# Optimization experiments

Hardware: AMD Instinct MI355X
Metric: run time of the kernel (lower is better)

## Reference

```python
import jax, jax.numpy as jnp
import numpy as np

D_MODEL = 768
HEADS = 12
D_HEAD = D_MODEL // HEADS
D_DYNA = 768
EPS = 1e-5
B, SP, SI = 16, 256, 1024


def _layernorm(x, g, b):
    mu = jnp.mean(x, axis=-1, keepdims=True)
    var = jnp.var(x, axis=-1, keepdims=True)
    return (x - mu) * jax.lax.rsqrt(var + EPS) * g + b


def _mha(q, k, v, wq, bq, wk, bk, wv, bv, wo, bo):
    # weights stored [d_in, d_out]; torch Linear math y = x @ W^T + b is
    # equivalent with transposed storage.
    B_ = q.shape[0]
    qh = (q @ wq + bq).reshape(B_, -1, HEADS, D_HEAD)
    kh = (k @ wk + bk).reshape(B_, -1, HEADS, D_HEAD)
    vh = (v @ wv + bv).reshape(B_, -1, HEADS, D_HEAD)
    scores = jnp.einsum('bqhd,bkhd->bhqk', qh, kh) / np.sqrt(D_HEAD).astype(np.float32)
    attn = jax.nn.softmax(scores, axis=-1)  # dropout disabled (eval)
    out = jnp.einsum('bhqk,bkhd->bqhd', attn, vh).reshape(B_, -1, D_MODEL)
    return out @ wo + bo


def setup_inputs() -> dict:
    key = jax.random.key(0)
    ks = iter(jax.random.split(key, 40))
    s = 0.02
    d = {
        'image': jax.random.normal(next(ks), (B, SI, D_MODEL), jnp.float32),
        'prompt': jax.random.normal(next(ks), (B, SP, D_MODEL), jnp.float32),
        'posi': jax.random.normal(next(ks), (B, SI, D_MODEL), jnp.float32),
        'posp': jax.random.normal(next(ks), (B, SP, D_MODEL), jnp.float32),
    }
    for ln in ('ln_p1', 'ln_p2', 'ln_p3', 'ln_i1'):
        d[ln + '_g'] = jnp.ones((D_MODEL,), jnp.float32)
        d[ln + '_b'] = jnp.zeros((D_MODEL,), jnp.float32)
    for pre in ('pp', 'pi'):
        for nm in ('q', 'k', 'v', 'o'):
            d[f'{pre}_w{nm}'] = s * jax.random.normal(next(ks), (D_MODEL, D_MODEL), jnp.float32)
            d[f'{pre}_b{nm}'] = jnp.zeros((D_MODEL,), jnp.float32)
    d['ff_w1'] = s * jax.random.normal(next(ks), (D_MODEL, D_MODEL), jnp.float32)
    d['ff_b1'] = jnp.zeros((D_MODEL,), jnp.float32)
    d['ff_w2'] = s * jax.random.normal(next(ks), (D_MODEL, D_DYNA), jnp.float32)
    d['ff_b2'] = jnp.zeros((D_DYNA,), jnp.float32)
    return d


def reference(image, prompt, posi, posp,
              ln_p1_g, ln_p1_b, ln_p2_g, ln_p2_b, ln_p3_g, ln_p3_b, ln_i1_g, ln_i1_b,
              pp_wq, pp_bq, pp_wk, pp_bk, pp_wv, pp_bv, pp_wo, pp_bo,
              pi_wq, pi_bq, pi_wk, pi_bk, pi_wv, pi_bv, pi_wo, pi_bo,
              ff_w1, ff_b1, ff_w2, ff_b2):
    prompt0 = prompt + posp
    xp = _layernorm(prompt0, ln_p1_g, ln_p1_b)
    xp = _mha(xp, xp, xp, pp_wq, pp_bq, pp_wk, pp_bk, pp_wv, pp_bv, pp_wo, pp_bo)
    prompt = prompt + xp  # dropout_p1 is identity in eval
    xp = _layernorm(prompt + prompt0, ln_p2_g, ln_p2_b)
    xi = _layernorm(image + posi, ln_i1_g, ln_i1_b)
    xp = _mha(xp, xi, xi, pi_wq, pi_bq, pi_wk, pi_bk, pi_wv, pi_bv, pi_wo, pi_bo)
    prompt = prompt + xp  # dropout_p2 identity
    xp = _layernorm(prompt + prompt0, ln_p3_g, ln_p3_b)
    xp = jax.nn.relu(xp @ ff_w1 + ff_b1) @ ff_w2 + ff_b2
    return xp
```

## Files before the change

kernel.cpp:

```cpp
#include <hip/hip_runtime.h>
#include <hip/hip_bf16.h>
#include <stdint.h>
#include <math.h>

#define D_MODEL 768
#define HEADS 12
#define D_HEAD 64
#define BATCH 16
#define SP 256
#define SI 1024
#define NP (BATCH * SP)
#define NI (BATCH * SI)

#define GLOBAL_AS __attribute__((address_space(1)))
#define LDS_AS    __attribute__((address_space(3)))

typedef __attribute__((ext_vector_type(8))) short  frag_ab;
typedef __attribute__((ext_vector_type(4))) float  frag_cd;

static __device__ __forceinline__ ushort f2bf(float f) {
  __hip_bfloat16 h = __float2bfloat16(f);
  return *(ushort*)&h;
}
static __device__ __forceinline__ float bf2f(ushort u) {
  return __bfloat162float(*(__hip_bfloat16*)&u);
}

__global__ void detect_kernel(const uint32_t* probe, int* flags) {
  if (threadIdx.x == 0) {
    flags[0] = (probe[0] == 0x3F803F80u) ? 1 : 0;
    flags[1] = 0;
    flags[2] = 1;
  }
}

struct ConvEntry { const void* src; float* dst; int n; };
struct ConvTable { ConvEntry e[24]; int cnt; };

__global__ __launch_bounds__(256) void convert_kernel(ConvTable t, const int* flag) {
  const bool isbf = (*flag != 0);
  for (int e = 0; e < t.cnt; e++) {
    const int n = t.e[e].n;
    float* __restrict__ dst = t.e[e].dst;
    if (isbf) {
      const __hip_bfloat16* s = (const __hip_bfloat16*)t.e[e].src;
      for (int i = blockIdx.x * blockDim.x + threadIdx.x; i < n; i += gridDim.x * blockDim.x)
        dst[i] = __bfloat162float(s[i]);
    } else {
      const float* s = (const float*)t.e[e].src;
      for (int i = blockIdx.x * blockDim.x + threadIdx.x; i < n; i += gridDim.x * blockDim.x)
        dst[i] = s[i];
    }
  }
}

struct TW { const void* src[10]; ushort* dst[10]; };

__global__ __launch_bounds__(256) void transpose_w_kernel(TW t, const int* flag) {
  __shared__ float tile[32][33];
  const bool isbf = (*flag != 0);
  const int tx = threadIdx.x, ty = threadIdx.y;
  const int x0 = blockIdx.x * 32, y0 = blockIdx.y * 32;
  const void* src = t.src[blockIdx.z];
  ushort* dst = t.dst[blockIdx.z];
#pragma unroll
  for (int i = 0; i < 4; i++) {
    const int y = y0 + ty + i * 8;
    float v;
    if (isbf) v = __bfloat162float(((const __hip_bfloat16*)src)[(size_t)y * 768 + x0 + tx]);
    else      v = ((const float*)src)[(size_t)y * 768 + x0 + tx];
    tile[ty + i * 8][tx] = v;
  }
  __syncthreads();
#pragma unroll
  for (int i = 0; i < 4; i++) {
    const int row = x0 + ty + i * 8;
    const int col = y0 + tx;
    dst[(size_t)row * 768 + col] = f2bf(tile[tx][ty + i * 8]);
  }
}

__global__ __launch_bounds__(192) void add_ln_kernel(
    const void* a, const void* b,
    const float* __restrict__ g, const float* __restrict__ be,
    float* __restrict__ sum_out, ushort* __restrict__ ln_out, const int* flag) {
  const int row = blockIdx.x;
  const int tid = threadIdx.x;
  const size_t base = (size_t)row * D_MODEL;
  const int c0 = tid * 4;
  const bool isbf = (*flag != 0);
  float x[4];
  if (isbf) {
    const uint2 ua = *(const uint2*)((const ushort*)a + base + c0);
    const uint2 ub = *(const uint2*)((const ushort*)b + base + c0);
    const ushort* pa = (const ushort*)&ua;
    const ushort* pb = (const ushort*)&ub;
#pragma unroll
    for (int t = 0; t < 4; t++) x[t] = bf2f(pa[t]) + bf2f(pb[t]);
  } else {
    const float4 fa = *(const float4*)((const float*)a + base + c0);
    const float4 fb = *(const float4*)((const float*)b + base + c0);
    x[0] = fa.x + fb.x; x[1] = fa.y + fb.y; x[2] = fa.z + fb.z; x[3] = fa.w + fb.w;
  }
  if (sum_out) {
    float4 s4; s4.x = x[0]; s4.y = x[1]; s4.z = x[2]; s4.w = x[3];
    *(float4*)&sum_out[base + c0] = s4;
  }
  __shared__ float rs[192], rq[192];
  __shared__ float stats[2];
  rs[tid] = x[0] + x[1] + x[2] + x[3];
  rq[tid] = x[0]*x[0] + x[1]*x[1] + x[2]*x[2] + x[3]*x[3];
  __syncthreads();
  if (tid < 64) {
    float s = rs[tid] + rs[tid + 64] + rs[tid + 128];
    float q = rq[tid] + rq[tid + 64] + rq[tid + 128];
#pragma unroll
    for (int o = 32; o > 0; o >>= 1) { s += __shfl_down(s, o); q += __shfl_down(q, o); }
    if (tid == 0) {
      const float mu  = s * (1.0f / D_MODEL);
      const float var = q * (1.0f / D_MODEL) - mu * mu;
      stats[0] = mu;
      stats[1] = rsqrtf(var + 1e-5f);
    }
  }
  __syncthreads();
  const float mu = stats[0], inv = stats[1];
  const float4 gv = *(const float4*)&g[c0];
  const float4 bv = *(const float4*)&be[c0];
  uint2 ou;
  ushort* oe = (ushort*)&ou;
  oe[0] = f2bf((x[0] - mu) * inv * gv.x + bv.x);
  oe[1] = f2bf((x[1] - mu) * inv * gv.y + bv.y);
  oe[2] = f2bf((x[2] - mu) * inv * gv.z + bv.z);
  oe[3] = f2bf((x[3] - mu) * inv * gv.w + bv.w);
  *(uint2*)(ln_out + base + c0) = ou;
}

__global__ __launch_bounds__(256) void gemm_bt(
    const ushort* __restrict__ A, const ushort* __restrict__ Bt,
    const float* __restrict__ bias, const float* __restrict__ resid,
    void* __restrict__ C, int relu, const int* outbf) {
  __shared__ ushort As[128 * 32];
  __shared__ ushort Bs[128 * 32];
  const int tid  = threadIdx.x;
  const int lane = tid & 63;
  const int w    = tid >> 6;
  const int wr   = w >> 1, wc = w & 1;
  const int ml   = lane & 15, kq = lane >> 4;
  const int m0   = blockIdx.y * 128, n0 = blockIdx.x * 128;

  frag_cd acc[4][4] = {};

  for (int k0 = 0; k0 < 768; k0 += 32) {
#pragma unroll
    for (int i = 0; i < 2; i++) {
      const int seg = w * 2 + i;
      const int r   = seg * 16 + (lane >> 2);
      const int kof = k0 + (lane & 3) * 8;
      const ushort* ga = A  + (size_t)(m0 + r) * 768 + kof;
      const ushort* gb = Bt + (size_t)(n0 + r) * 768 + kof;
      __builtin_amdgcn_global_load_lds((const GLOBAL_AS void*)ga,
          (LDS_AS void*)((LDS_AS ushort*)As + seg * 512), 16, 0, 0);
      __builtin_amdgcn_global_load_lds((const GLOBAL_AS void*)gb,
          (LDS_AS void*)((LDS_AS ushort*)Bs + seg * 512), 16, 0, 0);
    }
    __syncthreads();

    frag_ab af[4], bf[4];
#pragma unroll
    for (int t = 0; t < 4; t++) {
      af[t] = *(const frag_ab*)&As[(wr * 64 + t * 16 + ml) * 32 + kq * 8];
      bf[t] = *(const frag_ab*)&Bs[(wc * 64 + t * 16 + ml) * 32 + kq * 8];
    }
#pragma unroll
    for (int mt = 0; mt < 4; mt++)
#pragma unroll
      for (int nt = 0; nt < 4; nt++)
        acc[mt][nt] = __builtin_amdgcn_mfma_f32_16x16x32_bf16(
            af[mt], bf[nt], acc[mt][nt], 0, 0, 0);
    __syncthreads();
  }

  const bool obf = (outbf != nullptr) && (*outbf != 0);
#pragma unroll
  for (int mt = 0; mt < 4; mt++) {
#pragma unroll
    for (int nt = 0; nt < 4; nt++) {
      const int row0 = m0 + wr * 64 + mt * 16 + kq * 4;
      const int col  = n0 + wc * 64 + nt * 16 + ml;
      const float bc = bias[col];
#pragma unroll
      for (int r = 0; r < 4; r++) {
        float v = acc[mt][nt][r] + bc;
        if (resid) v += resid[(size_t)(row0 + r) * 768 + col];
        if (relu) v = fmaxf(v, 0.f);
        if (obf) {
          ((ushort*)C)[(size_t)(row0 + r) * 768 + col] = f2bf(v);
        } else {
          ((float*)C)[(size_t)(row0 + r) * 768 + col] = v;
        }
      }
    }
  }
}

struct MOut { ushort* o[3]; ushort* vT; int vsub; int shift; };

__global__ __launch_bounds__(256) void gemm_multi(
    const ushort* __restrict__ A, const ushort* __restrict__ Bt,
    const float* __restrict__ bias, MOut mo) {
  __shared__ ushort As[128 * 32];
  __shared__ ushort Bs[128 * 32];
  const int tid  = threadIdx.x;
  const int lane = tid & 63;
  const int w    = tid >> 6;
  const int wr   = w >> 1, wc = w & 1;
  const int ml   = lane & 15, kq = lane >> 4;
  const int m0   = blockIdx.y * 128, n0 = blockIdx.x * 128;

  frag_cd acc[4][4] = {};

  for (int k0 = 0; k0 < 768; k0 += 32) {
#pragma unroll
    for (int i = 0; i < 2; i++) {
      const int seg = w * 2 + i;
      const int r   = seg * 16 + (lane >> 2);
      const int kof = k0 + (lane & 3) * 8;
      const ushort* ga = A  + (size_t)(m0 + r) * 768 + kof;
      const ushort* gb = Bt + (size_t)(n0 + r) * 768 + kof;
      __builtin_amdgcn_global_load_lds((const GLOBAL_AS void*)ga,
          (LDS_AS void*)((LDS_AS ushort*)As + seg * 512), 16, 0, 0);
      __builtin_amdgcn_global_load_lds((const GLOBAL_AS void*)gb,
          (LDS_AS void*)((LDS_AS ushort*)Bs + seg * 512), 16, 0, 0);
    }
    __syncthreads();

    frag_ab af[4], bf[4];
#pragma unroll
    for (int t = 0; t < 4; t++) {
      af[t] = *(const frag_ab*)&As[(wr * 64 + t * 16 + ml) * 32 + kq * 8];
      bf[t] = *(const frag_ab*)&Bs[(wc * 64 + t * 16 + ml) * 32 + kq * 8];
    }
#pragma unroll
    for (int mt = 0; mt < 4; mt++)
#pragma unroll
      for (int nt = 0; nt < 4; nt++)
        acc[mt][nt] = __builtin_amdgcn_mfma_f32_16x16x32_bf16(
            af[mt], bf[nt], acc[mt][nt], 0, 0, 0);
    __syncthreads();
  }

  const int sub = n0 / 768;
  const int mask = (1 << mo.shift) - 1;
#pragma unroll
  for (int mt = 0; mt < 4; mt++) {
#pragma unroll
    for (int nt = 0; nt < 4; nt++) {
      const int row0 = m0 + wr * 64 + mt * 16 + kq * 4;
      const int col  = n0 + wc * 64 + nt * 16 + ml;
      const float bc = bias[col];
      if (sub == mo.vsub) {
        const int hcol = col - sub * 768;
        const int hh = hcol >> 6, dd = hcol & 63;
        const int bb = row0 >> mo.shift;
        const int j0 = row0 & mask;
        uint2 pack;
        ushort* pe = (ushort*)&pack;
#pragma unroll
        for (int r = 0; r < 4; r++) pe[r] = f2bf(acc[mt][nt][r] + bc);
        *(uint2*)(mo.vT + ((((size_t)(bb * HEADS + hh) << 6) + dd) << mo.shift) + j0) = pack;
      } else {
        ushort* out = mo.o[sub];
        const int cl = col - sub * 768;
#pragma unroll
        for (int r = 0; r < 4; r++)
          out[(size_t)(row0 + r) * 768 + cl] = f2bf(acc[mt][nt][r] + bc);
      }
    }
  }
}

#define FS 68
__global__ __launch_bounds__(256) void fattn_mfma(
    const ushort* __restrict__ Q, const ushort* __restrict__ Kp,
    const ushort* __restrict__ vT, ushort* __restrict__ O, int Skv) {
  __shared__ __align__(16) ushort Qs[64 * FS];
  __shared__ __align__(16) ushort Ks[64 * FS];
  __shared__ __align__(16) ushort Vt[64 * FS];
  __shared__ __align__(16) ushort Ps[64 * FS];
  const int tid  = threadIdx.x;
  const int lane = tid & 63, w = tid >> 6;
  const int ml   = lane & 15, kq = lane >> 4;
  const int bid = blockIdx.x;
  const int g8  = bid & 7;
  const int qt  = (bid >> 3) & 3;
  const int g   = (bid >> 5) * 8 + g8;
  const int h   = g % HEADS;
  const int b   = g / HEADS;
  const int q0  = qt * 64;
  const ushort* Qb  = Q  + ((size_t)b * SP + q0) * D_MODEL + h * D_HEAD;
  const ushort* Kb  = Kp + (size_t)b * Skv * D_MODEL + h * D_HEAD;
  const ushort* vTb = vT + (size_t)g * 64 * Skv;

  for (int c = tid; c < 512; c += 256) {
    const int r = c >> 3, p = c & 7;
    *(uint4*)&Qs[r * FS + p * 8] = *(const uint4*)(Qb + (size_t)r * D_MODEL + p * 8);
  }
  __syncthreads();
  frag_ab qa[2];
#pragma unroll
  for (int kc = 0; kc < 2; kc++)
    qa[kc] = *(const frag_ab*)&Qs[(w * 16 + ml) * FS + kc * 32 + kq * 8];

  frag_cd oc[4] = {};
  float m_i[4], l_i[4];
#pragma unroll
  for (int r = 0; r < 4; r++) { m_i[r] = -1e30f; l_i[r] = 0.f; }
  const float SCL = 0.125f * 1.44269504f;

  for (int j0 = 0; j0 < Skv; j0 += 64) {
    __syncthreads();
    for (int c = tid; c < 512; c += 256) {
      const int r = c >> 3, p = c & 7;
      *(uint4*)&Ks[r * FS + p * 8] = *(const uint4*)(Kb + (size_t)(j0 + r) * D_MODEL + p * 8);
      *(uint4*)&Vt[r * FS + p * 8] = *(const uint4*)(vTb + (size_t)r * Skv + j0 + p * 8);
    }
    __syncthreads();

    frag_cd sc[4] = {};
#pragma unroll
    for (int nt = 0; nt < 4; nt++)
#pragma unroll
      for (int kc = 0; kc < 2; kc++) {
        const frag_ab bfr = *(const frag_ab*)&Ks[(nt * 16 + ml) * FS + kc * 32 + kq * 8];
        sc[nt] = __builtin_amdgcn_mfma_f32_16x16x32_bf16(qa[kc], bfr, sc[nt], 0, 0, 0);
      }
#pragma unroll
    for (int nt = 0; nt < 4; nt++)
#pragma unroll
      for (int r = 0; r < 4; r++) sc[nt][r] *= SCL;

    float al[4];
#pragma unroll
    for (int r = 0; r < 4; r++) {
      float mx = fmaxf(fmaxf(sc[0][r], sc[1][r]), fmaxf(sc[2][r], sc[3][r]));
#pragma unroll
      for (int m = 1; m < 16; m <<= 1) mx = fmaxf(mx, __shfl_xor(mx, m, 16));
      const float mnew = fmaxf(m_i[r], mx);
      al[r] = exp2f(m_i[r] - mnew);
      float p[4], s = 0.f;
#pragma unroll
      for (int nt = 0; nt < 4; nt++) { p[nt] = exp2f(sc[nt][r] - mnew); s += p[nt]; }
#pragma unroll
      for (int m = 1; m < 16; m <<= 1) s += __shfl_xor(s, m, 16);
      l_i[r] = l_i[r] * al[r] + s;
      m_i[r] = mnew;
      const int prow = (w * 16 + kq * 4 + r) * FS;
#pragma unroll
      for (int nt = 0; nt < 4; nt++) Ps[prow + nt * 16 + ml] = f2bf(p[nt]);
    }
#pragma unroll
    for (int dt = 0; dt < 4; dt++)
#pragma unroll
      for (int r = 0; r < 4; r++) oc[dt][r] *= al[r];

#pragma unroll
    for (int kc = 0; kc < 2; kc++) {
      const frag_ab pa = *(const frag_ab*)&Ps[(w * 16 + ml) * FS + kc * 32 + kq * 8];
#pragma unroll
      for (int dt = 0; dt < 4; dt++) {
        const frag_ab vb = *(const frag_ab*)&Vt[(dt * 16 + ml) * FS + kc * 32 + kq * 8];
        oc[dt] = __builtin_amdgcn_mfma_f32_16x16x32_bf16(pa, vb, oc[dt], 0, 0, 0);
      }
    }
  }

  float inv[4];
#pragma unroll
  for (int r = 0; r < 4; r++) inv[r] = 1.0f / l_i[r];
#pragma unroll
  for (int dt = 0; dt < 4; dt++)
#pragma unroll
    for (int r = 0; r < 4; r++)
      O[((size_t)b * SP + q0 + w * 16 + kq * 4 + r) * D_MODEL + h * D_HEAD + dt * 16 + ml] =
          f2bf(oc[dt][r] * inv[r]);
}

extern "C" void kernel_launch(void* const* d_in, const int* in_sizes, int n_in,
                              void* d_out, int out_size, void* d_ws, size_t ws_size,
                              hipStream_t stream) {
  (void)in_sizes; (void)n_in; (void)out_size;
  char* base = (char*)d_ws;
  int* flags = (int*)d_ws;
  size_t off = 256;
  auto alloc = [&](size_t bytes) -> char* {
    char* p = base + off;
    off = (off + bytes + 255) & ~(size_t)255;
    return p;
  };
  const size_t WB = (size_t)768 * 768 * 2;
  ushort* Wt[10];
  for (int i = 0; i < 10; i++) Wt[i] = (ushort*)alloc(WB);
  float* biasF[10];
  for (int i = 0; i < 10; i++) biasF[i] = (float*)alloc(768 * 4);
  float* lnF[8];
  for (int i = 0; i < 8; i++) lnF[i] = (float*)alloc(768 * 4);
  float* promptF = (float*)alloc((size_t)NP * 768 * 4);
  float* prompt0 = (float*)alloc((size_t)NP * 768 * 4);
  float* cur     = (float*)alloc((size_t)NP * 768 * 4);
  ushort* q_bf   = (ushort*)alloc((size_t)NP * 768 * 2);
  ushort* k_bf   = (ushort*)alloc((size_t)NI * 768 * 2);
  ushort* xln_bf = (ushort*)alloc((size_t)NP * 768 * 2);
  ushort* xi_bf  = (ushort*)alloc((size_t)NI * 768 * 2);
  ushort* obuf_bf = (ushort*)alloc((size_t)NP * 768 * 2);
  ushort* ffn1_bf = (ushort*)alloc((size_t)NP * 768 * 2);
  ushort* vT_s   = (ushort*)alloc((size_t)BATCH * HEADS * 64 * SP * 2);
  ushort* vT_c   = (ushort*)alloc((size_t)BATCH * HEADS * 64 * SI * 2);
  if (ws_size < off) return;

  const int* flag  = flags;
  const int* oflag = flags + 2;

  detect_kernel<<<1, 64, 0, stream>>>((const uint32_t*)d_in[4], flags);

  const int widx[10] = {12, 14, 16, 18, 20, 22, 24, 26, 28, 30};
  const int bidx[10] = {13, 15, 17, 19, 21, 23, 25, 27, 29, 31};

  TW tw{};
  for (int i = 0; i < 10; i++) { tw.src[i] = d_in[widx[i]]; tw.dst[i] = Wt[i]; }
  transpose_w_kernel<<<dim3(24, 24, 10), dim3(32, 8), 0, stream>>>(tw, flag);

  ConvTable t{};
  int c = 0;
  for (int i = 0; i < 10; i++) t.e[c++] = { d_in[bidx[i]], biasF[i], 768 };
  for (int i = 0; i < 8;  i++) t.e[c++] = { d_in[4 + i], lnF[i], 768 };
  t.e[c++] = { d_in[1], promptF, NP * 768 };
  t.cnt = c;
  convert_kernel<<<1024, 256, 0, stream>>>(t, flag);

  float* G1 = lnF[0], *B1 = lnF[1];
  float* G2 = lnF[2], *B2 = lnF[3];
  float* G3 = lnF[4], *B3 = lnF[5];
  float* Gi = lnF[6], *Bi = lnF[7];

  const dim3 gp(6, NP / 128);
  const int attn_grid = BATCH * HEADS * (SP / 64);

  add_ln_kernel<<<NP, 192, 0, stream>>>(d_in[1], d_in[3], G1, B1, prompt0, xln_bf, flag);
  MOut moS{};
  moS.o[0] = q_bf; moS.o[1] = k_bf; moS.o[2] = nullptr;
  moS.vT = vT_s; moS.vsub = 2; moS.shift = 8;
  gemm_multi<<<dim3(18, NP / 128), 256, 0, stream>>>(xln_bf, Wt[0], biasF[0], moS);
  fattn_mfma<<<attn_grid, 256, 0, stream>>>(q_bf, k_bf, vT_s, obuf_bf, SP);
  gemm_bt<<<gp, 256, 0, stream>>>(obuf_bf, Wt[3], biasF[3], promptF, cur, 0, nullptr);
  add_ln_kernel<<<NP, 192, 0, stream>>>(cur, prompt0, G2, B2, nullptr, xln_bf, flags + 1);
  add_ln_kernel<<<NI, 192, 0, stream>>>(d_in[0], d_in[2], Gi, Bi, nullptr, xi_bf, flag);
  gemm_bt<<<gp, 256, 0, stream>>>(xln_bf, Wt[4], biasF[4], nullptr, q_bf, 0, oflag);
  MOut moC{};
  moC.o[0] = k_bf; moC.o[1] = nullptr; moC.o[2] = nullptr;
  moC.vT = vT_c; moC.vsub = 1; moC.shift = 10;
  gemm_multi<<<dim3(12, NI / 128), 256, 0, stream>>>(xi_bf, Wt[5], biasF[5], moC);
  fattn_mfma<<<attn_grid, 256, 0, stream>>>(q_bf, k_bf, vT_c, obuf_bf, SI);
  gemm_bt<<<gp, 256, 0, stream>>>(obuf_bf, Wt[7], biasF[7], cur, cur, 0, nullptr);
  add_ln_kernel<<<NP, 192, 0, stream>>>(cur, prompt0, G3, B3, nullptr, xln_bf, flags + 1);
  gemm_bt<<<gp, 256, 0, stream>>>(xln_bf, Wt[8], biasF[8], nullptr, ffn1_bf, 1, oflag);
  gemm_bt<<<gp, 256, 0, stream>>>(ffn1_bf, Wt[9], biasF[9], nullptr, d_out, 0, flag);
}
```

Before: 560.8 us.

## Merge prep kernels, batch LN and QKV GEMMs, use 64-row tiles for small GEMMs

Replaces the detect, convert and transpose kernels with one prep kernel that reads the dtype probe inline. The prompt-to-float copy is dropped because the residual GEMM now reads the raw prompt directly. The two input LayerNorms run in one launch, and the self-attention and cross-attention QKV projections share one mega GEMM launch with a grouped block swizzle. The 4096-row GEMMs switch to 64-row tiles so more blocks fill the CUs. The aim is fewer launches and better occupancy on small GEMMs, at the cost of more branching per block and less reuse per tile.

```diff
diff --git a/kernel.cpp b/kernel.cpp
--- a/kernel.cpp
+++ b/kernel.cpp
@@ -25,86 +25,82 @@
 static __device__ __forceinline__ float bf2f(ushort u) {
   return __bfloat162float(*(__hip_bfloat16*)&u);
 }
-
-__global__ void detect_kernel(const uint32_t* probe, int* flags) {
-  if (threadIdx.x == 0) {
-    flags[0] = (probe[0] == 0x3F803F80u) ? 1 : 0;
-    flags[1] = 0;
-    flags[2] = 1;
-  }
-}
-
-struct ConvEntry { const void* src; float* dst; int n; };
-struct ConvTable { ConvEntry e[24]; int cnt; };
-
-__global__ __launch_bounds__(256) void convert_kernel(ConvTable t, const int* flag) {
-  const bool isbf = (*flag != 0);
-  for (int e = 0; e < t.cnt; e++) {
-    const int n = t.e[e].n;
-    float* __restrict__ dst = t.e[e].dst;
-    if (isbf) {
-      const __hip_bfloat16* s = (const __hip_bfloat16*)t.e[e].src;
-      for (int i = blockIdx.x * blockDim.x + threadIdx.x; i < n; i += gridDim.x * blockDim.x)
-        dst[i] = __bfloat162float(s[i]);
-    } else {
-      const float* s = (const float*)t.e[e].src;
-      for (int i = blockIdx.x * blockDim.x + threadIdx.x; i < n; i += gridDim.x * blockDim.x)
-        dst[i] = s[i];
-    }
-  }
-}
-
-struct TW { const void* src[10]; ushort* dst[10]; };
-
-__global__ __launch_bounds__(256) void transpose_w_kernel(TW t, const int* flag) {
-  __shared__ float tile[32][33];
-  const bool isbf = (*flag != 0);
-  const int tx = threadIdx.x, ty = threadIdx.y;
-  const int x0 = blockIdx.x * 32, y0 = blockIdx.y * 32;
-  const void* src = t.src[blockIdx.z];
-  ushort* dst = t.dst[blockIdx.z];
-#pragma unroll
-  for (int i = 0; i < 4; i++) {
-    const int y = y0 + ty + i * 8;
-    float v;
-    if (isbf) v = __bfloat162float(((const __hip_bfloat16*)src)[(size_t)y * 768 + x0 + tx]);
-    else      v = ((const float*)src)[(size_t)y * 768 + x0 + tx];
-    tile[ty + i * 8][tx] = v;
-  }
-  __syncthreads();
-#pragma unroll
-  for (int i = 0; i < 4; i++) {
-    const int row = x0 + ty + i * 8;
-    const int col = y0 + tx;
-    dst[(size_t)row * 768 + col] = f2bf(tile[tx][ty + i * 8]);
-  }
-}
-
-__global__ __launch_bounds__(192) void add_ln_kernel(
-    const void* a, const void* b,
-    const float* __restrict__ g, const float* __restrict__ be,
-    float* __restrict__ sum_out, ushort* __restrict__ ln_out, const int* flag) {
-  const int row = blockIdx.x;
+static __device__ __forceinline__ bool probe_bf(const uint32_t* p) {
+  return p[0] == 0x3F803F80u;
+}
+
+struct Prep {
+  const void* wsrc[10]; ushort* wdst[10];
+  const void* vsrc[18]; float* vdst;
+};
+
+__global__ __launch_bounds__(256) void prep_kernel(Prep p, const uint32_t* probe) {
+  const bool isbf = probe_bf(probe);
+  const int z = blockIdx.z;
+  if (z < 10) {
+    __shared__ float tile[32][33];
+    const int tx = threadIdx.x & 31, ty = threadIdx.x >> 5;
+    const int x0 = blockIdx.x * 32, y0 = blockIdx.y * 32;
+    const void* src = p.wsrc[z];
+    ushort* dst = p.wdst[z];
+#pragma unroll
+    for (int i = 0; i < 4; i++) {
+      const int y = y0 + ty + i * 8;
+      float v;
+      if (isbf) v = bf2f(((const ushort*)src)[(size_t)y * 768 + x0 + tx]);
+      else      v = ((const float*)src)[(size_t)y * 768 + x0 + tx];
+      tile[ty + i * 8][tx] = v;
+    }
+    __syncthreads();
+#pragma unroll
+    for (int i = 0; i < 4; i++) {
+      const int row = x0 + ty + i * 8;
+      const int col = y0 + tx;
+      dst[(size_t)row * 768 + col] = f2bf(tile[tx][ty + i * 8]);
+    }
+  } else {
+    const int idx = (blockIdx.y * 24 + blockIdx.x) * 256 + threadIdx.x;
+    if (idx < 18 * 768) {
+      const int e = idx / 768, i = idx - e * 768;
+      float v;
+      if (isbf) v = bf2f(((const ushort*)p.vsrc[e])[i]);
+      else      v = ((const float*)p.vsrc[e])[i];
+      p.vdst[idx] = v;
+    }
+  }
+}
+
+struct LNJob {
+  const void* a; const void* b;
+  const float* g; const float* be;
+  float* sum_out; ushort* ln_out;
+  int nrows; int abf;
+};
+
+__global__ __launch_bounds__(192) void add_ln2(LNJob J0, LNJob J1, const uint32_t* probe) {
+  int row = blockIdx.x;
+  LNJob j = (row < J0.nrows) ? J0 : J1;
+  if (row >= J0.nrows) row -= J0.nrows;
   const int tid = threadIdx.x;
   const size_t base = (size_t)row * D_MODEL;
   const int c0 = tid * 4;
-  const bool isbf = (*flag != 0);
+  const bool isbf = j.abf && probe_bf(probe);
   float x[4];
   if (isbf) {
-    const uint2 ua = *(const uint2*)((const ushort*)a + base + c0);
-    const uint2 ub = *(const uint2*)((const ushort*)b + base + c0);
+    const uint2 ua = *(const uint2*)((const ushort*)j.a + base + c0);
+    const uint2 ub = *(const uint2*)((const ushort*)j.b + base + c0);
     const ushort* pa = (const ushort*)&ua;
     const ushort* pb = (const ushort*)&ub;
 #pragma unroll
     for (int t = 0; t < 4; t++) x[t] = bf2f(pa[t]) + bf2f(pb[t]);
   } else {
-    const float4 fa = *(const float4*)((const float*)a + base + c0);
-    const float4 fb = *(const float4*)((const float*)b + base + c0);
+    const float4 fa = *(const float4*)((const float*)j.a + base + c0);
+    const float4 fb = *(const float4*)((const float*)j.b + base + c0);
     x[0] = fa.x + fb.x; x[1] = fa.y + fb.y; x[2] = fa.z + fb.z; x[3] = fa.w + fb.w;
   }
-  if (sum_out) {
+  if (j.sum_out) {
     float4 s4; s4.x = x[0]; s4.y = x[1]; s4.z = x[2]; s4.w = x[3];
-    *(float4*)&sum_out[base + c0] = s4;
+    *(float4*)&j.sum_out[base + c0] = s4;
   }
   __shared__ float rs[192], rq[192];
   __shared__ float stats[2];
@@ -125,29 +121,115 @@
   }
   __syncthreads();
   const float mu = stats[0], inv = stats[1];
-  const float4 gv = *(const float4*)&g[c0];
-  const float4 bv = *(const float4*)&be[c0];
+  const float4 gv = *(const float4*)&j.g[c0];
+  const float4 bv = *(const float4*)&j.be[c0];
   uint2 ou;
   ushort* oe = (ushort*)&ou;
   oe[0] = f2bf((x[0] - mu) * inv * gv.x + bv.x);
   oe[1] = f2bf((x[1] - mu) * inv * gv.y + bv.y);
   oe[2] = f2bf((x[2] - mu) * inv * gv.z + bv.z);
   oe[3] = f2bf((x[3] - mu) * inv * gv.w + bv.w);
-  *(uint2*)(ln_out + base + c0) = ou;
-}
-
-__global__ __launch_bounds__(256) void gemm_bt(
+  *(uint2*)(j.ln_out + base + c0) = ou;
+}
+
+template<int BM>
+__global__ __launch_bounds__(256) void gemm_k(
     const ushort* __restrict__ A, const ushort* __restrict__ Bt,
-    const float* __restrict__ bias, const float* __restrict__ resid,
-    void* __restrict__ C, int relu, const int* outbf) {
+    const float* __restrict__ bias,
+    const void* __restrict__ resid, int rmode,
+    void* __restrict__ C, int relu, int omode,
+    const uint32_t* __restrict__ probe, int X) {
+  __shared__ ushort As[BM * 32];
+  __shared__ ushort Bs[128 * 32];
+  const int tid  = threadIdx.x;
+  const int lane = tid & 63, w = tid >> 6;
+  const int wr = w >> 1, wc = w & 1;
+  const int ml = lane & 15, kq = lane >> 4;
+  const int bid = blockIdx.x;
+  const int rest = bid >> 3;
+  const int x = rest % X, y = (bid & 7) + 8 * (rest / X);
+  const int m0 = y * BM, n0 = x * 128;
+  constexpr int MT   = BM / 32;
+  constexpr int ASEG = BM / 16;
+  constexpr int NSEG = (ASEG + 8) / 4;
+
+  frag_cd acc[MT][4] = {};
+
+  for (int k0 = 0; k0 < 768; k0 += 32) {
+#pragma unroll
+    for (int i = 0; i < NSEG; i++) {
+      const int s = w + i * 4;
+      const bool isA = (s < ASEG);
+      const int seg = isA ? s : (s - ASEG);
+      const int r   = seg * 16 + (lane >> 2);
+      const int kof = k0 + (lane & 3) * 8;
+      if (isA)
+        __builtin_amdgcn_global_load_lds((const GLOBAL_AS void*)(A + (size_t)(m0 + r) * 768 + kof),
+            (LDS_AS void*)((LDS_AS ushort*)As + seg * 512), 16, 0, 0);
+      else
+        __builtin_amdgcn_global_load_lds((const GLOBAL_AS void*)(Bt + (size_t)(n0 + r) * 768 + kof),
+            (LDS_AS void*)((LDS_AS ushort*)Bs + seg * 512), 16, 0, 0);
+    }
+    __syncthreads();
+
+    frag_ab af[MT], bf4[4];
+#pragma unroll
+    for (int t = 0; t < MT; t++)
+      af[t] = *(const frag_ab*)&As[(wr * (BM / 2) + t * 16 + ml) * 32 + kq * 8];
+#pragma unroll
+    for (int t = 0; t < 4; t++)
+      bf4[t] = *(const frag_ab*)&Bs[(wc * 64 + t * 16 + ml) * 32 + kq * 8];
+#pragma unroll
+    for (int mt = 0; mt < MT; mt++)
+#pragma unroll
+      for (int nt = 0; nt < 4; nt++)
+        acc[mt][nt] = __builtin_amdgcn_mfma_f32_16x16x32_bf16(
+            af[mt], bf4[nt], acc[mt][nt], 0, 0, 0);
+    __syncthreads();
+  }
+
+  const bool obf = (omode == 1) || (omode == 2 && probe_bf(probe));
+  const bool rbf = (rmode == 2) && probe_bf(probe);
+#pragma unroll
+  for (int mt = 0; mt < MT; mt++) {
+#pragma unroll
+    for (int nt = 0; nt < 4; nt++) {
+      const int row0 = m0 + wr * (BM / 2) + mt * 16 + kq * 4;
+      const int col  = n0 + wc * 64 + nt * 16 + ml;
+      const float bc = bias[col];
+#pragma unroll
+      for (int r = 0; r < 4; r++) {
+        const size_t off = (size_t)(row0 + r) * 768 + col;
+        float v = acc[mt][nt][r] + bc;
+        if (rmode != 0)
+          v += rbf ? bf2f(((const ushort*)resid)[off]) : ((const float*)resid)[off];
+        if (relu) v = fmaxf(v, 0.f);
+        if (obf) ((ushort*)C)[off] = f2bf(v);
+        else     ((float*)C)[off]  = v;
+      }
+    }
+  }
+}
+
+struct GJob {
+  const ushort* A; const ushort* Bt; const float* bias;
+  ushort* o0; ushort* o1; ushort* vT;
+  int X; int vsub; int shift;
+};
+
+__global__ __launch_bounds__(256) void gemm_mega(GJob J0, GJob J1, int n0blocks) {
   __shared__ ushort As[128 * 32];
   __shared__ ushort Bs[128 * 32];
+  int bid = blockIdx.x;
+  GJob j = (bid < n0blocks) ? J0 : J1;
+  if (bid >= n0blocks) bid -= n0blocks;
   const int tid  = threadIdx.x;
-  const int lane = tid & 63;
-  const int w    = tid >> 6;
-  const int wr   = w >> 1, wc = w & 1;
-  const int ml   = lane & 15, kq = lane >> 4;
-  const int m0   = blockIdx.y * 128, n0 = blockIdx.x * 128;
+  const int lane = tid & 63, w = tid >> 6;
+  const int wr = w >> 1, wc = w & 1;
+  const int ml = lane & 15, kq = lane >> 4;
+  const int rest = bid >> 3;
+  const int x = rest % j.X, y = (bid & 7) + 8 * (rest / j.X);
+  const int m0 = y * 128, n0 = x * 128;
 
   frag_cd acc[4][4] = {};
 
@@ -157,120 +239,49 @@
       const int seg = w * 2 + i;
       const int r   = seg * 16 + (lane >> 2);
       const int kof = k0 + (lane & 3) * 8;
-      const ushort* ga = A  + (size_t)(m0 + r) * 768 + kof;
-      const ushort* gb = Bt + (size_t)(n0 + r) * 768 + kof;
-      __builtin_amdgcn_global_load_lds((const GLOBAL_AS void*)ga,
+      __builtin_amdgcn_global_load_lds((const GLOBAL_AS void*)(j.A + (size_t)(m0 + r) * 768 + kof),
           (LDS_AS void*)((LDS_AS ushort*)As + seg * 512), 16, 0, 0);
-      __builtin_amdgcn_global_load_lds((const GLOBAL_AS void*)gb,
+      __builtin_amdgcn_global_load_lds((const GLOBAL_AS void*)(j.Bt + (size_t)(n0 + r) * 768 + kof),
           (LDS_AS void*)((LDS_AS ushort*)Bs + seg * 512), 16, 0, 0);
     }
     __syncthreads();
 
-    frag_ab af[4], bf[4];
+    frag_ab af[4], bf4[4];
 #pragma unroll
     for (int t = 0; t < 4; t++) {
-      af[t] = *(const frag_ab*)&As[(wr * 64 + t * 16 + ml) * 32 + kq * 8];
-      bf[t] = *(const frag_ab*)&Bs[(wc * 64 + t * 16 + ml) * 32 + kq * 8];
+      af[t]  = *(const frag_ab*)&As[(wr * 64 + t * 16 + ml) * 32 + kq * 8];
+      bf4[t] = *(const frag_ab*)&Bs[(wc * 64 + t * 16 + ml) * 32 + kq * 8];
     }
 #pragma unroll
     for (int mt = 0; mt < 4; mt++)
 #pragma unroll
       for (int nt = 0; nt < 4; nt++)
         acc[mt][nt] = __builtin_amdgcn_mfma_f32_16x16x32_bf16(
-            af[mt], bf[nt], acc[mt][nt], 0, 0, 0);
-    __syncthreads();
-  }
-
-  const bool obf = (outbf != nullptr) && (*outbf != 0);
+            af[mt], bf4[nt], acc[mt][nt], 0, 0, 0);
+    __syncthreads();
+  }
+
+  const int sub  = x / 6;
+  const int mask = (1 << j.shift) - 1;
 #pragma unroll
   for (int mt = 0; mt < 4; mt++) {
 #pragma unroll
     for (int nt = 0; nt < 4; nt++) {
       const int row0 = m0 + wr * 64 + mt * 16 + kq * 4;
       const int col  = n0 + wc * 64 + nt * 16 + ml;
-      const float bc = bias[col];
-#pragma unroll
-      for (int r = 0; r < 4; r++) {
-        float v = acc[mt][nt][r] + bc;
-        if (resid) v += resid[(size_t)(row0 + r) * 768 + col];
-        if (relu) v = fmaxf(v, 0.f);
-        if (obf) {
-          ((ushort*)C)[(size_t)(row0 + r) * 768 + col] = f2bf(v);
-        } else {
-          ((float*)C)[(size_t)(row0 + r) * 768 + col] = v;
-        }
-      }
-    }
-  }
-}
-
-struct MOut { ushort* o[3]; ushort* vT; int vsub; int shift; };
-
-__global__ __launch_bounds__(256) void gemm_multi(
-    const ushort* __restrict__ A, const ushort* __restrict__ Bt,
-    const float* __restrict__ bias, MOut mo) {
-  __shared__ ushort As[128 * 32];
-  __shared__ ushort Bs[128 * 32];
-  const int tid  = threadIdx.x;
-  const int lane = tid & 63;
-  const int w    = tid >> 6;
-  const int wr   = w >> 1, wc = w & 1;
-  const int ml   = lane & 15, kq = lane >> 4;
-  const int m0   = blockIdx.y * 128, n0 = blockIdx.x * 128;
-
-  frag_cd acc[4][4] = {};
-
-  for (int k0 = 0; k0 < 768; k0 += 32) {
-#pragma unroll
-    for (int i = 0; i < 2; i++) {
-      const int seg = w * 2 + i;
-      const int r   = seg * 16 + (lane >> 2);
-      const int kof = k0 + (lane & 3) * 8;
-      const ushort* ga = A  + (size_t)(m0 + r) * 768 + kof;
-      const ushort* gb = Bt + (size_t)(n0 + r) * 768 + kof;
-      __builtin_amdgcn_global_load_lds((const GLOBAL_AS void*)ga,
-          (LDS_AS void*)((LDS_AS ushort*)As + seg * 512), 16, 0, 0);
-      __builtin_amdgcn_global_load_lds((const GLOBAL_AS void*)gb,
-          (LDS_AS void*)((LDS_AS ushort*)Bs + seg * 512), 16, 0, 0);
-    }
-    __syncthreads();
-
-    frag_ab af[4], bf[4];
-#pragma unroll
-    for (int t = 0; t < 4; t++) {
-      af[t] = *(const frag_ab*)&As[(wr * 64 + t * 16 + ml) * 32 + kq * 8];
-      bf[t] = *(const frag_ab*)&Bs[(wc * 64 + t * 16 + ml) * 32 + kq * 8];
-    }
-#pragma unroll
-    for (int mt = 0; mt < 4; mt++)
-#pragma unroll
-      for (int nt = 0; nt < 4; nt++)
-        acc[mt][nt] = __builtin_amdgcn_mfma_f32_16x16x32_bf16(
-            af[mt], bf[nt], acc[mt][nt], 0, 0, 0);
-    __syncthreads();
-  }
-
-  const int sub = n0 / 768;
-  const int mask = (1 << mo.shift) - 1;
-#pragma unroll
-  for (int mt = 0; mt < 4; mt++) {
-#pragma unroll
-    for (int nt = 0; nt < 4; nt++) {
-      const int row0 = m0 + wr * 64 + mt * 16 + kq * 4;
-      const int col  = n0 + wc * 64 + nt * 16 + ml;
-      const float bc = bias[col];
-      if (sub == mo.vsub) {
+      const float bc = j.bias[col];
+      if (sub == j.vsub) {
         const int hcol = col - sub * 768;
         const int hh = hcol >> 6, dd = hcol & 63;
-        const int bb = row0 >> mo.shift;
-        const int j0 = row0 & mask;
+        const int bb = row0 >> j.shift;
+        const int jj = row0 & mask;
         uint2 pack;
         ushort* pe = (ushort*)&pack;
 #pragma unroll
         for (int r = 0; r < 4; r++) pe[r] = f2bf(acc[mt][nt][r] + bc);
-        *(uint2*)(mo.vT + ((((size_t)(bb * HEADS + hh) << 6) + dd) << mo.shift) + j0) = pack;
+        *(uint2*)(j.vT + ((((size_t)(bb * HEADS + hh) << 6) + dd) << j.shift) + jj) = pack;
       } else {
-        ushort* out = mo.o[sub];
+        ushort* out = (sub == 0) ? j.o0 : j.o1;
         const int cl = col - sub * 768;
 #pragma unroll
         for (int r = 0; r < 4; r++)
@@ -391,7 +402,6 @@
                               hipStream_t stream) {
   (void)in_sizes; (void)n_in; (void)out_size;
   char* base = (char*)d_ws;
-  int* flags = (int*)d_ws;
   size_t off = 256;
   auto alloc = [&](size_t bytes) -> char* {
     char* p = base + off;
@@ -401,15 +411,15 @@
   const size_t WB = (size_t)768 * 768 * 2;
   ushort* Wt[10];
   for (int i = 0; i < 10; i++) Wt[i] = (ushort*)alloc(WB);
+  float* vecs = (float*)alloc(18 * 768 * 4);
   float* biasF[10];
-  for (int i = 0; i < 10; i++) biasF[i] = (float*)alloc(768 * 4);
-  float* lnF[8];
-  for (int i = 0; i < 8; i++) lnF[i] = (float*)alloc(768 * 4);
-  float* promptF = (float*)alloc((size_t)NP * 768 * 4);
+  for (int i = 0; i < 10; i++) biasF[i] = vecs + i * 768;
+  float* lnF = vecs + 10 * 768;
   float* prompt0 = (float*)alloc((size_t)NP * 768 * 4);
   float* cur     = (float*)alloc((size_t)NP * 768 * 4);
   ushort* q_bf   = (ushort*)alloc((size_t)NP * 768 * 2);
-  ushort* k_bf   = (ushort*)alloc((size_t)NI * 768 * 2);
+  ushort* k_s    = (ushort*)alloc((size_t)NP * 768 * 2);
+  ushort* k_c    = (ushort*)alloc((size_t)NI * 768 * 2);
   ushort* xln_bf = (ushort*)alloc((size_t)NP * 768 * 2);
   ushort* xi_bf  = (ushort*)alloc((size_t)NI * 768 * 2);
   ushort* obuf_bf = (ushort*)alloc((size_t)NP * 768 * 2);
@@ -418,51 +428,53 @@
   ushort* vT_c   = (ushort*)alloc((size_t)BATCH * HEADS * 64 * SI * 2);
   if (ws_size < off) return;
 
-  const int* flag  = flags;
-  const int* oflag = flags + 2;
-
-  detect_kernel<<<1, 64, 0, stream>>>((const uint32_t*)d_in[4], flags);
-
+  const uint32_t* probe = (const uint32_t*)d_in[4];
   const int widx[10] = {12, 14, 16, 18, 20, 22, 24, 26, 28, 30};
   const int bidx[10] = {13, 15, 17, 19, 21, 23, 25, 27, 29, 31};
 
-  TW tw{};
-  for (int i = 0; i < 10; i++) { tw.src[i] = d_in[widx[i]]; tw.dst[i] = Wt[i]; }
-  transpose_w_kernel<<<dim3(24, 24, 10), dim3(32, 8), 0, stream>>>(tw, flag);
-
-  ConvTable t{};
-  int c = 0;
-  for (int i = 0; i < 10; i++) t.e[c++] = { d_in[bidx[i]], biasF[i], 768 };
-  for (int i = 0; i < 8;  i++) t.e[c++] = { d_in[4 + i], lnF[i], 768 };
-  t.e[c++] = { d_in[1], promptF, NP * 768 };
-  t.cnt = c;
-  convert_kernel<<<1024, 256, 0, stream>>>(t, flag);
-
-  float* G1 = lnF[0], *B1 = lnF[1];
-  float* G2 = lnF[2], *B2 = lnF[3];
-  float* G3 = lnF[4], *B3 = lnF[5];
-  float* Gi = lnF[6], *Bi = lnF[7];
-
-  const dim3 gp(6, NP / 128);
-  const int attn_grid = BATCH * HEADS * (SP / 64);
-
-  add_ln_kernel<<<NP, 192, 0, stream>>>(d_in[1], d_in[3], G1, B1, prompt0, xln_bf, flag);
-  MOut moS{};
-  moS.o[0] = q_bf; moS.o[1] = k_bf; moS.o[2] = nullptr;
-  moS.vT = vT_s; moS.vsub = 2; moS.shift = 8;
-  gemm_multi<<<dim3(18, NP / 128), 256, 0, stream>>>(xln_bf, Wt[0], biasF[0], moS);
-  fattn_mfma<<<attn_grid, 256, 0, stream>>>(q_bf, k_bf, vT_s, obuf_bf, SP);
-  gemm_bt<<<gp, 256, 0, stream>>>(obuf_bf, Wt[3], biasF[3], promptF, cur, 0, nullptr);
-  add_ln_kernel<<<NP, 192, 0, stream>>>(cur, prompt0, G2, B2, nullptr, xln_bf, flags + 1);
-  add_ln_kernel<<<NI, 192, 0, stream>>>(d_in[0], d_in[2], Gi, Bi, nullptr, xi_bf, flag);
-  gemm_bt<<<gp, 256, 0, stream>>>(xln_bf, Wt[4], biasF[4], nullptr, q_bf, 0, oflag);
-  MOut moC{};
-  moC.o[0] = k_bf; moC.o[1] = nullptr; moC.o[2] = nullptr;
-  moC.vT = vT_c; moC.vsub = 1; moC.shift = 10;
-  gemm_multi<<<dim3(12, NI / 128), 256, 0, stream>>>(xi_bf, Wt[5], biasF[5], moC);
-  fattn_mfma<<<attn_grid, 256, 0, stream>>>(q_bf, k_bf, vT_c, obuf_bf, SI);
-  gemm_bt<<<gp, 256, 0, stream>>>(obuf_bf, Wt[7], biasF[7], cur, cur, 0, nullptr);
-  add_ln_kernel<<<NP, 192, 0, stream>>>(cur, prompt0, G3, B3, nullptr, xln_bf, flags + 1);
-  gemm_bt<<<gp, 256, 0, stream>>>(xln_bf, Wt[8], biasF[8], nullptr, ffn1_bf, 1, oflag);
-  gemm_bt<<<gp, 256, 0, stream>>>(ffn1_bf, Wt[9], biasF[9], nullptr, d_out, 0, flag);
-}
+  Prep pr{};
+  for (int i = 0; i < 10; i++) { pr.wsrc[i] = d_in[widx[i]]; pr.wdst[i] = Wt[i]; }
+  for (int i = 0; i < 10; i++) pr.vsrc[i] = d_in[bidx[i]];
+  for (int i = 0; i < 8;  i++) pr.vsrc[10 + i] = d_in[4 + i];
+  pr.vdst = vecs;
+  prep_kernel<<<dim3(24, 24, 11), 256, 0, stream>>>(pr, probe);
+
+  float* G1 = lnF + 0 * 768, *B1 = lnF + 1 * 768;
+  float* G2 = lnF + 2 * 768, *B2 = lnF + 3 * 768;
+  float* G3 = lnF + 4 * 768, *B3 = lnF + 5 * 768;
+  float* Gi = lnF + 6 * 768, *Bi = lnF + 7 * 768;
+
+  LNJob L0{d_in[1], d_in[3], G1, B1, prompt0, xln_bf, NP, 1};
+  LNJob Li{d_in[0], d_in[2], Gi, Bi, nullptr, xi_bf,  NI, 1};
+  add_ln2<<<NP + NI, 192, 0, stream>>>(L0, Li, probe);
+
+  GJob js{xln_bf, Wt[0], biasF[0], q_bf, k_s, vT_s, 18, 2, 8};
+  GJob jc{xi_bf,  Wt[5], biasF[5], k_c,  nullptr, vT_c, 12, 1, 10};
+  gemm_mega<<<576 + 1536, 256, 0, stream>>>(js, jc, 576);
+
+  fattn_mfma<<<BATCH * HEADS * (SP / 64), 256, 0, stream>>>(q_bf, k_s, vT_s, obuf_bf, SP);
+
+  gemm_k<64><<<6 * 64, 256, 0, stream>>>(obuf_bf, Wt[3], biasF[3],
+      d_in[1], 2, cur, 0, 0, probe, 6);
+
+  LNJob L2{cur, prompt0, G2, B2, nullptr, xln_bf, NP, 0};
+  LNJob Lz{}; Lz.nrows = 0;
+  add_ln2<<<NP, 192, 0, stream>>>(L2, Lz, probe);
+
+  gemm_k<64><<<6 * 64, 256, 0, stream>>>(xln_bf, Wt[4], biasF[4],
+      nullptr, 0, q_bf, 0, 1, probe, 6);
+
+  fattn_mfma<<<BATCH * HEADS * (SP / 64), 256, 0, stream>>>(q_bf, k_c, vT_c, obuf_bf, SI);
+
+  gemm_k<64><<<6 * 64, 256, 0, stream>>>(obuf_bf, Wt[7], biasF[7],
+      cur, 1, cur, 0, 0, probe, 6);
+
+  LNJob L3{cur, prompt0, G3, B3, nullptr, xln_bf, NP, 0};
+  add_ln2<<<NP, 192, 0, stream>>>(L3, Lz, probe);
+
+  gemm_k<64><<<6 * 64, 256, 0, stream>>>(xln_bf, Wt[8], biasF[8],
+      nullptr, 0, ffn1_bf, 1, 1, probe, 6);
+
+  gemm_k<64><<<6 * 64, 256, 0, stream>>>(ffn1_bf, Wt[9], biasF[9],
+      nullptr, 0, d_out, 0, 2, probe, 6);
+}
```

Result: faster. 490.2 us (-12.6%).
